# Kernel tuning notes

Hardware: AMD Instinct MI355X
Metric: run time of the kernel (lower is better)

## Reference

```python
import jax, jax.numpy as jnp
import numpy as np

B, N, D, H, L = 2, 2048, 512, 8, 2
HD = D // H


def setup_inputs() -> dict:
    key = jax.random.key(0)
    ks = jax.random.split(key, 8)
    s = 0.02
    return {
        "inputs_embeds": jax.random.normal(ks[0], (B, N, D), jnp.float32),
        "pos_emb": jax.random.normal(ks[1], (N, D), jnp.float32) * s,
        "c_attn_w": jax.random.normal(ks[2], (L, D, 3 * D), jnp.float32) * s,
        "c_attn_b": jnp.zeros((L, 3 * D), jnp.float32),
        "out_w": jax.random.normal(ks[3], (L, D, D), jnp.float32) * s,
        "out_b": jnp.zeros((L, D), jnp.float32),
        "ln1_g": jnp.ones((L, D), jnp.float32),
        "ln1_b": jnp.zeros((L, D), jnp.float32),
        "c_fc_w": jax.random.normal(ks[4], (L, D, 4 * D), jnp.float32) * s,
        "c_fc_b": jnp.zeros((L, 4 * D), jnp.float32),
        "c_proj_w": jax.random.normal(ks[5], (L, 4 * D, D), jnp.float32) * s,
        "c_proj_b": jnp.zeros((L, D), jnp.float32),
        "ln2_g": jnp.ones((L, D), jnp.float32),
        "ln2_b": jnp.zeros((L, D), jnp.float32),
    }


def _layernorm(x, g, b, eps=1e-5):
    mu = jnp.mean(x, axis=-1, keepdims=True)
    var = jnp.mean(jnp.square(x - mu), axis=-1, keepdims=True)
    return (x - mu) * jax.lax.rsqrt(var + eps) * g + b


def _gelu_new(x):
    # NewGELUActivation: tanh approximation
    return 0.5 * x * (1.0 + jnp.tanh(jnp.sqrt(2.0 / jnp.pi) * (x + 0.044715 * x ** 3)))


def _attention(x, w_qkv, b_qkv, w_out, b_out, self_mask):
    qkv = x @ w_qkv + b_qkv                      # [B,N,3D]
    q, k, v = jnp.split(qkv, 3, axis=-1)
    def heads(t):
        return t.reshape(B, N, H, HD).transpose(0, 2, 1, 3)  # [B,H,N,HD]
    q, k, v = heads(q), heads(k), heads(v)
    scores = jnp.einsum('bhqd,bhkd->bhqk', q, k) / jnp.sqrt(jnp.float32(HD))
    neg = jnp.finfo(scores.dtype).min
    scores = jnp.where(self_mask, scores, neg)   # exclude-self mask
    attn = jax.nn.softmax(scores, axis=-1)
    o = jnp.einsum('bhqk,bhkd->bhqd', attn, v)
    o = o.transpose(0, 2, 1, 3).reshape(B, N, D)
    return o @ w_out + b_out


def reference(inputs_embeds, pos_emb, c_attn_w, c_attn_b, out_w, out_b,
              ln1_g, ln1_b, c_fc_w, c_fc_b, c_proj_w, c_proj_b, ln2_g, ln2_b):
    self_mask = ~jnp.eye(N, dtype=bool)[None, None]  # [1,1,N,N]
    h = inputs_embeds + pos_emb[None]
    for l in range(L):
        res = h
        x = _layernorm(h, ln1_g[l], ln1_b[l])
        h = _attention(x, c_attn_w[l], c_attn_b[l], out_w[l], out_b[l], self_mask) + res
        res = h
        x = _layernorm(h, ln2_g[l], ln2_b[l])
        x = _gelu_new(x @ c_fc_w[l] + c_fc_b[l])
        h = (x @ c_proj_w[l] + c_proj_b[l]) + res
    return h
```

## Files before the change

kernel.cpp:

```cpp
#include <hip/hip_runtime.h>
#include <hip/hip_bf16.h>
#include <math.h>

#define BB 2
#define NN 2048
#define DD 512
#define HH 8
#define LL 2
#define TT (BB*NN)

typedef short short8 __attribute__((ext_vector_type(8)));
typedef float floatx4 __attribute__((ext_vector_type(4)));

__device__ __forceinline__ unsigned short f2b(float v) {
    union { float f; unsigned u; } x; x.f = v;
    unsigned r = x.u + 0x7fff + ((x.u >> 16) & 1);
    return (unsigned short)(r >> 16);
}

__global__ __launch_bounds__(256) void k_embed(const float* __restrict__ emb,
                                               const float* __restrict__ pos,
                                               float* __restrict__ h) {
    int i = blockIdx.x * 256 + threadIdx.x;
    h[i] = emb[i] + pos[i & (NN * DD - 1)];
}

__global__ __launch_bounds__(256) void k_ln(const float* __restrict__ hin,
                                            unsigned short* __restrict__ xout,
                                            const float* __restrict__ g,
                                            const float* __restrict__ b) {
    __shared__ float red[4];
    __shared__ float bc1, bc2;
    int t = blockIdx.x;
    int tid = threadIdx.x;
    int lane = tid & 63, wv = tid >> 6;
    const float* row = hin + (size_t)t * DD;
    float v0 = row[tid];
    float v1 = row[tid + 256];

    float s = v0 + v1;
#pragma unroll
    for (int o = 32; o; o >>= 1) s += __shfl_down(s, o, 64);
    if (lane == 0) red[wv] = s;
    __syncthreads();
    if (tid == 0) bc1 = (red[0] + red[1] + red[2] + red[3]) * (1.0f / DD);
    __syncthreads();
    float mu = bc1;
    float d0 = v0 - mu, d1 = v1 - mu;
    s = d0 * d0 + d1 * d1;
#pragma unroll
    for (int o = 32; o; o >>= 1) s += __shfl_down(s, o, 64);
    if (lane == 0) red[wv] = s;
    __syncthreads();
    if (tid == 0) bc2 = (red[0] + red[1] + red[2] + red[3]) * (1.0f / DD);
    __syncthreads();
    float rstd = rsqrtf(bc2 + 1e-5f);
    xout[(size_t)t * DD + tid]       = f2b(d0 * rstd * g[tid] + b[tid]);
    xout[(size_t)t * DD + tid + 256] = f2b(d1 * rstd * g[tid + 256] + b[tid + 256]);
}

__device__ __forceinline__ float gelu_new(float v) {
    const float c = 0.7978845608028654f;
    float u = c * (v + 0.044715f * v * v * v);
    return 0.5f * v * (1.0f + tanhf(u));
}

#define PL 3145728
__global__ __launch_bounds__(256) void k_wt_all(const float* __restrict__ c_attn_w,
                                                const float* __restrict__ out_w,
                                                const float* __restrict__ c_fc_w,
                                                const float* __restrict__ c_proj_w,
                                                unsigned short* __restrict__ wbuf) {
    __shared__ unsigned short t[64][72];
    int bx = blockIdx.x;
    int l = bx / 768;
    int r = bx - l * 768;
    const float* W; unsigned short* WT; int K, N;
    if (r < 192)      { W = c_attn_w + (size_t)l * 512 * 1536; WT = wbuf + (size_t)l * PL;           K = 512;  N = 1536; }
    else if (r < 256) { r -= 192; W = out_w  + (size_t)l * 512 * 512;  WT = wbuf + (size_t)l * PL + 786432;  K = 512;  N = 512; }
    else if (r < 512) { r -= 256; W = c_fc_w + (size_t)l * 512 * 2048; WT = wbuf + (size_t)l * PL + 1048576; K = 512;  N = 2048; }
    else              { r -= 512; W = c_proj_w + (size_t)l * 2048 * 512; WT = wbuf + (size_t)l * PL + 2097152; K = 2048; N = 512; }
    int tiles_n = N >> 6;
    int n0 = (r % tiles_n) * 64, k0 = (r / tiles_n) * 64;

    int tid = threadIdx.x;
    int rr = tid >> 2;
    int c0 = (tid & 3) * 16;
    const float* src = W + (size_t)(k0 + rr) * N + n0 + c0;
#pragma unroll
    for (int u = 0; u < 4; u++) {
        float4 v = *(const float4*)&src[u * 4];
        t[c0 + u * 4 + 0][rr] = f2b(v.x);
        t[c0 + u * 4 + 1][rr] = f2b(v.y);
        t[c0 + u * 4 + 2][rr] = f2b(v.z);
        t[c0 + u * 4 + 3][rr] = f2b(v.w);
    }
    __syncthreads();
    unsigned short* dst = WT + (size_t)(n0 + rr) * K + k0 + c0;
#pragma unroll
    for (int u = 0; u < 4; u++)
        *(uint2*)&dst[u * 4] = *(const uint2*)&t[rr][c0 + u * 4];
}

template <int ACT, int RES, int BF16OUT>
__global__ __launch_bounds__(256) void k_mgemm(const unsigned short* __restrict__ Ab,
                                               const unsigned short* __restrict__ Bt,
                                               const float* __restrict__ bias,
                                               const float* __restrict__ Rp,
                                               float* __restrict__ Cp,
                                               unsigned short* __restrict__ Cb,
                                               int K, int N) {
    __shared__ unsigned short Als[8 * 512];
    __shared__ unsigned short Bls[8 * 512];

    int tid = threadIdx.x;
    int l = tid & 63, w = tid >> 6;
    int wm = w >> 1, wn = w & 1;
    int m0 = blockIdx.y * 128, n0 = blockIdx.x * 128;
    int lr = l & 15;
    int lk = (l >> 4) * 8;

    const unsigned short* Ap0 = Ab + (size_t)(m0 + (w * 2 + 0) * 16 + lr) * K + lk;
    const unsigned short* Ap1 = Ab + (size_t)(m0 + (w * 2 + 1) * 16 + lr) * K + lk;
    const unsigned short* Bp0 = Bt + (size_t)(n0 + (w * 2 + 0) * 16 + lr) * K + lk;
    const unsigned short* Bp1 = Bt + (size_t)(n0 + (w * 2 + 1) * 16 + lr) * K + lk;

    floatx4 acc[4][4];
#pragma unroll
    for (int i = 0; i < 4; i++)
#pragma unroll
        for (int j = 0; j < 4; j++) acc[i][j] = (floatx4){0.f, 0.f, 0.f, 0.f};

    uint4 ra0 = *(const uint4*)Ap0;
    uint4 ra1 = *(const uint4*)Ap1;
    uint4 rb0 = *(const uint4*)Bp0;
    uint4 rb1 = *(const uint4*)Bp1;

    for (int k0 = 0; k0 < K; k0 += 32) {
        __syncthreads();
        *(uint4*)&Als[(w * 2 + 0) * 512 + l * 8] = ra0;
        *(uint4*)&Als[(w * 2 + 1) * 512 + l * 8] = ra1;
        *(uint4*)&Bls[(w * 2 + 0) * 512 + l * 8] = rb0;
        *(uint4*)&Bls[(w * 2 + 1) * 512 + l * 8] = rb1;
        __syncthreads();
        if (k0 + 32 < K) {
            ra0 = *(const uint4*)(Ap0 + k0 + 32);
            ra1 = *(const uint4*)(Ap1 + k0 + 32);
            rb0 = *(const uint4*)(Bp0 + k0 + 32);
            rb1 = *(const uint4*)(Bp1 + k0 + 32);
        }
        short8 a[4], b[4];
#pragma unroll
        for (int i = 0; i < 4; i++) {
            a[i] = *(const short8*)&Als[(wm * 4 + i) * 512 + l * 8];
            b[i] = *(const short8*)&Bls[(wn * 4 + i) * 512 + l * 8];
        }
#pragma unroll
        for (int i = 0; i < 4; i++)
#pragma unroll
            for (int j = 0; j < 4; j++)
                acc[i][j] = __builtin_amdgcn_mfma_f32_16x16x32_bf16(a[i], b[j], acc[i][j], 0, 0, 0);
    }

    int col_in = l & 15, rquad = (l >> 4) * 4;
#pragma unroll
    for (int i = 0; i < 4; i++) {
        int gm_base = m0 + wm * 64 + i * 16 + rquad;
#pragma unroll
        for (int j = 0; j < 4; j++) {
            int gn = n0 + wn * 64 + j * 16 + col_in;
            float bv = bias[gn];
#pragma unroll
            for (int r = 0; r < 4; r++) {
                size_t off = (size_t)(gm_base + r) * N + gn;
                float v = acc[i][j][r] + bv;
                if (ACT) v = gelu_new(v);
                if (RES) v += Rp[off];
                if (BF16OUT) Cb[off] = f2b(v);
                else Cp[off] = v;
            }
        }
    }
}

__global__ __launch_bounds__(256) void k_attn_mfma(const unsigned short* __restrict__ qkv,
                                                   unsigned short* __restrict__ xatt) {
    __shared__ unsigned short Ks[64 * 72];
    __shared__ unsigned short Vt[64 * 72];
    __shared__ unsigned short Pls[64 * 72];

    int qt = blockIdx.x, hd = blockIdx.y, b = blockIdx.z;
    int tid = threadIdx.x;
    int l = tid & 63, w = tid >> 6;
    int lr = l & 15, quad = l >> 4;

    const size_t base = (size_t)b * NN * 1536;

    short8 qf[2];
    {
        const unsigned short* qrow = qkv + base + (size_t)(qt * 64 + w * 16 + lr) * 1536 + hd * 64;
        qf[0] = *(const short8*)&qrow[quad * 8];
        qf[1] = *(const short8*)&qrow[quad * 8 + 32];
    }

    floatx4 O[4];
#pragma unroll
    for (int jd = 0; jd < 4; jd++) O[jd] = (floatx4){0.f, 0.f, 0.f, 0.f};
    float lsum[4] = {0.f, 0.f, 0.f, 0.f};

    int sr = tid >> 2, sc = (tid & 3) * 16;
    int vk = (tid & 15) * 4, vd = (tid >> 4) * 4;
    const unsigned short* Kbase = qkv + base + 512 + hd * 64;
    const unsigned short* Vbase = qkv + base + 1024 + hd * 64;

    uint4 rk0, rk1;
    union { uint2 u; unsigned short s[4]; } rv[4];
    rk0 = *(const uint4*)&Kbase[(size_t)sr * 1536 + sc];
    rk1 = *(const uint4*)&Kbase[(size_t)sr * 1536 + sc + 8];
#pragma unroll
    for (int i = 0; i < 4; i++)
        rv[i].u = *(const uint2*)&Vbase[(size_t)(vk + i) * 1536 + vd];

    for (int kt = 0; kt < 32; kt++) {
        __syncthreads();
        *(uint4*)&Ks[sr * 72 + sc]     = rk0;
        *(uint4*)&Ks[sr * 72 + sc + 8] = rk1;
#pragma unroll
        for (int j = 0; j < 4; j++) {
            union { uint2 u; unsigned short s[4]; } pk;
            pk.s[0] = rv[0].s[j]; pk.s[1] = rv[1].s[j];
            pk.s[2] = rv[2].s[j]; pk.s[3] = rv[3].s[j];
            *(uint2*)&Vt[(vd + j) * 72 + vk] = pk.u;
        }
        __syncthreads();
        if (kt < 31) {
            int kn = (kt + 1) * 64;
            rk0 = *(const uint4*)&Kbase[(size_t)(kn + sr) * 1536 + sc];
            rk1 = *(const uint4*)&Kbase[(size_t)(kn + sr) * 1536 + sc + 8];
#pragma unroll
            for (int i = 0; i < 4; i++)
                rv[i].u = *(const uint2*)&Vbase[(size_t)(kn + vk + i) * 1536 + vd];
        }

        floatx4 s[4];
#pragma unroll
        for (int jn = 0; jn < 4; jn++) s[jn] = (floatx4){0.f, 0.f, 0.f, 0.f};
#pragma unroll
        for (int ss = 0; ss < 2; ss++)
#pragma unroll
            for (int jn = 0; jn < 4; jn++) {
                short8 bk = *(const short8*)&Ks[(jn * 16 + lr) * 72 + ss * 32 + quad * 8];
                s[jn] = __builtin_amdgcn_mfma_f32_16x16x32_bf16(qf[ss], bk, s[jn], 0, 0, 0);
            }

        float p[4][4];
#pragma unroll
        for (int jn = 0; jn < 4; jn++)
#pragma unroll
            for (int r = 0; r < 4; r++)
                p[jn][r] = __expf(s[jn][r] * 0.125f - 8.0f);
        if (kt == qt) {
            int m_base = w * 16 + quad * 4;
#pragma unroll
            for (int jn = 0; jn < 4; jn++)
#pragma unroll
                for (int r = 0; r < 4; r++)
                    if (m_base + r == jn * 16 + lr) p[jn][r] = 0.0f;
        }
#pragma unroll
        for (int jn = 0; jn < 4; jn++)
#pragma unroll
            for (int r = 0; r < 4; r++) {
                lsum[r] += p[jn][r];
                Pls[(w * 16 + quad * 4 + r) * 72 + jn * 16 + lr] = f2b(p[jn][r]);
            }

#pragma unroll
        for (int ss = 0; ss < 2; ss++) {
            short8 ap = *(const short8*)&Pls[(w * 16 + lr) * 72 + ss * 32 + quad * 8];
#pragma unroll
            for (int jd = 0; jd < 4; jd++) {
                short8 bv = *(const short8*)&Vt[(jd * 16 + lr) * 72 + ss * 32 + quad * 8];
                O[jd] = __builtin_amdgcn_mfma_f32_16x16x32_bf16(ap, bv, O[jd], 0, 0, 0);
            }
        }
    }

#pragma unroll
    for (int r = 0; r < 4; r++) {
#pragma unroll
        for (int msk = 1; msk < 16; msk <<= 1) lsum[r] += __shfl_xor(lsum[r], msk);
    }
#pragma unroll
    for (int r = 0; r < 4; r++) {
        float inv = 1.0f / lsum[r];
        size_t tok = (size_t)b * NN + qt * 64 + w * 16 + quad * 4 + r;
#pragma unroll
        for (int jd = 0; jd < 4; jd++)
            xatt[tok * DD + hd * 64 + jd * 16 + lr] = f2b(O[jd][r] * inv);
    }
}

__global__ __launch_bounds__(256) void k_copy(const float* __restrict__ h,
                                              float* __restrict__ out) {
    int i = blockIdx.x * 256 + threadIdx.x;
    out[i] = h[i];
}

extern "C" void kernel_launch(void* const* d_in, const int* in_sizes, int n_in,
                              void* d_out, int out_size, void* d_ws, size_t ws_size,
                              hipStream_t stream) {
    const float* emb      = (const float*)d_in[0];
    const float* pos      = (const float*)d_in[1];
    const float* c_attn_w = (const float*)d_in[2];
    const float* c_attn_b = (const float*)d_in[3];
    const float* out_w    = (const float*)d_in[4];
    const float* out_b    = (const float*)d_in[5];
    const float* ln1_g    = (const float*)d_in[6];
    const float* ln1_b    = (const float*)d_in[7];
    const float* c_fc_w   = (const float*)d_in[8];
    const float* c_fc_b   = (const float*)d_in[9];
    const float* c_proj_w = (const float*)d_in[10];
    const float* c_proj_b = (const float*)d_in[11];
    const float* ln2_g    = (const float*)d_in[12];
    const float* ln2_b    = (const float*)d_in[13];

    char* p = (char*)d_ws;
    float* h = (float*)p;                       p += (size_t)TT * DD * 4;
    unsigned short* act = (unsigned short*)p;   p += (size_t)TT * 2048 * 2;
    unsigned short* x = (unsigned short*)p;     p += (size_t)TT * DD * 2;
    unsigned short* xatt = (unsigned short*)p;  p += (size_t)TT * DD * 2;
    unsigned short* wbuf = (unsigned short*)p;

    unsigned short* qkvb = act;
    unsigned short* ffa  = act;
    float* out = (float*)d_out;

    k_embed<<<TT * DD / 256, 256, 0, stream>>>(emb, pos, h);
    k_wt_all<<<1536, 256, 0, stream>>>(c_attn_w, out_w, c_fc_w, c_proj_w, wbuf);

    for (int l = 0; l < LL; l++) {
        unsigned short* wqkv_t  = wbuf + (size_t)l * PL;
        unsigned short* wout_t  = wqkv_t + 786432;
        unsigned short* wfc_t   = wqkv_t + 1048576;
        unsigned short* wproj_t = wqkv_t + 2097152;

        k_ln<<<TT, 256, 0, stream>>>(h, x, ln1_g + l * DD, ln1_b + l * DD);
        k_mgemm<0, 0, 1><<<dim3(1536 / 128, TT / 128), 256, 0, stream>>>(
            x, wqkv_t, c_attn_b + l * 1536, nullptr, nullptr, qkvb, 512, 1536);
        k_attn_mfma<<<dim3(NN / 64, HH, BB), 256, 0, stream>>>(qkvb, xatt);
        k_mgemm<0, 1, 0><<<dim3(512 / 128, TT / 128), 256, 0, stream>>>(
            xatt, wout_t, out_b + l * 512, h, h, nullptr, 512, 512);
        k_ln<<<TT, 256, 0, stream>>>(h, x, ln2_g + l * DD, ln2_b + l * DD);
        k_mgemm<1, 0, 1><<<dim3(2048 / 128, TT / 128), 256, 0, stream>>>(
            x, wfc_t, c_fc_b + l * 2048, nullptr, nullptr, ffa, 512, 2048);
        k_mgemm<0, 1, 0><<<dim3(512 / 128, TT / 128), 256, 0, stream>>>(
            ffa, wproj_t, c_proj_b + l * 512, h, h, nullptr, 2048, 512);
    }

    k_copy<<<TT * DD / 256, 256, 0, stream>>>(h, out);
}
```

Before: 442.8 us.

## Double-buffer GEMM LDS with async loads, transpose attention scores, drop final copy

The GEMM mainloop now uses two LDS buffers. It prefetches the next K-slice straight into LDS with global_load_lds when that builtin exists, so each iteration needs one barrier instead of two and skips the register staging. The attention kernel computes the scores as K·Qᵀ, so each lane holds one query row. That lets P be written to LDS with vectorized stores and cuts the row-sum reduction to two shuffles. The last layer's projection GEMM writes directly to the output buffer, which removes the separate copy kernel. The main risk is whether the async LDS loads are correctly waited on before the barrier.

Result: slower. 462.2 us (+4.4%).

```diff
diff --git a/kernel.cpp b/kernel.cpp
--- a/kernel.cpp
+++ b/kernel.cpp
@@ -17,6 +17,17 @@
     unsigned r = x.u + 0x7fff + ((x.u >> 16) & 1);
     return (unsigned short)(r >> 16);
 }
+
+#if __has_builtin(__builtin_amdgcn_global_load_lds)
+#define HAVE_ASYNC 1
+__device__ __forceinline__ void g2l16(const void* g, void* l) {
+    __builtin_amdgcn_global_load_lds(
+        (const __attribute__((address_space(1))) unsigned int*)g,
+        (__attribute__((address_space(3))) unsigned int*)l, 16, 0, 0);
+}
+#else
+#define HAVE_ASYNC 0
+#endif
 
 __global__ __launch_bounds__(256) void k_embed(const float* __restrict__ emb,
                                                const float* __restrict__ pos,
@@ -110,8 +121,8 @@
                                                float* __restrict__ Cp,
                                                unsigned short* __restrict__ Cb,
                                                int K, int N) {
-    __shared__ unsigned short Als[8 * 512];
-    __shared__ unsigned short Bls[8 * 512];
+    __shared__ unsigned short Als[2][8 * 512];
+    __shared__ unsigned short Bls[2][8 * 512];
 
     int tid = threadIdx.x;
     int l = tid & 63, w = tid >> 6;
@@ -124,6 +135,8 @@
     const unsigned short* Ap1 = Ab + (size_t)(m0 + (w * 2 + 1) * 16 + lr) * K + lk;
     const unsigned short* Bp0 = Bt + (size_t)(n0 + (w * 2 + 0) * 16 + lr) * K + lk;
     const unsigned short* Bp1 = Bt + (size_t)(n0 + (w * 2 + 1) * 16 + lr) * K + lk;
+    int la0 = (w * 2 + 0) * 512 + l * 8;
+    int la1 = (w * 2 + 1) * 512 + l * 8;
 
     floatx4 acc[4][4];
 #pragma unroll
@@ -131,29 +144,41 @@
 #pragma unroll
         for (int j = 0; j < 4; j++) acc[i][j] = (floatx4){0.f, 0.f, 0.f, 0.f};
 
-    uint4 ra0 = *(const uint4*)Ap0;
-    uint4 ra1 = *(const uint4*)Ap1;
-    uint4 rb0 = *(const uint4*)Bp0;
-    uint4 rb1 = *(const uint4*)Bp1;
-
-    for (int k0 = 0; k0 < K; k0 += 32) {
+#if HAVE_ASYNC
+    g2l16(Ap0, &Als[0][la0]);
+    g2l16(Ap1, &Als[0][la1]);
+    g2l16(Bp0, &Bls[0][la0]);
+    g2l16(Bp1, &Bls[0][la1]);
+#else
+    *(uint4*)&Als[0][la0] = *(const uint4*)Ap0;
+    *(uint4*)&Als[0][la1] = *(const uint4*)Ap1;
+    *(uint4*)&Bls[0][la0] = *(const uint4*)Bp0;
+    *(uint4*)&Bls[0][la1] = *(const uint4*)Bp1;
+#endif
+
+    int nit = K >> 5;
+    for (int it = 0; it < nit; it++) {
+        int cur = it & 1;
         __syncthreads();
-        *(uint4*)&Als[(w * 2 + 0) * 512 + l * 8] = ra0;
-        *(uint4*)&Als[(w * 2 + 1) * 512 + l * 8] = ra1;
-        *(uint4*)&Bls[(w * 2 + 0) * 512 + l * 8] = rb0;
-        *(uint4*)&Bls[(w * 2 + 1) * 512 + l * 8] = rb1;
-        __syncthreads();
-        if (k0 + 32 < K) {
-            ra0 = *(const uint4*)(Ap0 + k0 + 32);
-            ra1 = *(const uint4*)(Ap1 + k0 + 32);
-            rb0 = *(const uint4*)(Bp0 + k0 + 32);
-            rb1 = *(const uint4*)(Bp1 + k0 + 32);
+        if (it + 1 < nit) {
+            int ko = (it + 1) << 5;
+#if HAVE_ASYNC
+            g2l16(Ap0 + ko, &Als[cur ^ 1][la0]);
+            g2l16(Ap1 + ko, &Als[cur ^ 1][la1]);
+            g2l16(Bp0 + ko, &Bls[cur ^ 1][la0]);
+            g2l16(Bp1 + ko, &Bls[cur ^ 1][la1]);
+#else
+            *(uint4*)&Als[cur ^ 1][la0] = *(const uint4*)(Ap0 + ko);
+            *(uint4*)&Als[cur ^ 1][la1] = *(const uint4*)(Ap1 + ko);
+            *(uint4*)&Bls[cur ^ 1][la0] = *(const uint4*)(Bp0 + ko);
+            *(uint4*)&Bls[cur ^ 1][la1] = *(const uint4*)(Bp1 + ko);
+#endif
         }
         short8 a[4], b[4];
 #pragma unroll
         for (int i = 0; i < 4; i++) {
-            a[i] = *(const short8*)&Als[(wm * 4 + i) * 512 + l * 8];
-            b[i] = *(const short8*)&Bls[(wn * 4 + i) * 512 + l * 8];
+            a[i] = *(const short8*)&Als[cur][(wm * 4 + i) * 512 + l * 8];
+            b[i] = *(const short8*)&Bls[cur][(wn * 4 + i) * 512 + l * 8];
         }
 #pragma unroll
         for (int i = 0; i < 4; i++)
@@ -206,7 +231,7 @@
     floatx4 O[4];
 #pragma unroll
     for (int jd = 0; jd < 4; jd++) O[jd] = (floatx4){0.f, 0.f, 0.f, 0.f};
-    float lsum[4] = {0.f, 0.f, 0.f, 0.f};
+    float lsum = 0.0f;
 
     int sr = tid >> 2, sc = (tid & 3) * 16;
     int vk = (tid & 15) * 4, vd = (tid >> 4) * 4;
@@ -249,31 +274,23 @@
         for (int ss = 0; ss < 2; ss++)
 #pragma unroll
             for (int jn = 0; jn < 4; jn++) {
-                short8 bk = *(const short8*)&Ks[(jn * 16 + lr) * 72 + ss * 32 + quad * 8];
-                s[jn] = __builtin_amdgcn_mfma_f32_16x16x32_bf16(qf[ss], bk, s[jn], 0, 0, 0);
+                short8 ak = *(const short8*)&Ks[(jn * 16 + lr) * 72 + ss * 32 + quad * 8];
+                s[jn] = __builtin_amdgcn_mfma_f32_16x16x32_bf16(ak, qf[ss], s[jn], 0, 0, 0);
             }
 
-        float p[4][4];
-#pragma unroll
-        for (int jn = 0; jn < 4; jn++)
-#pragma unroll
-            for (int r = 0; r < 4; r++)
-                p[jn][r] = __expf(s[jn][r] * 0.125f - 8.0f);
-        if (kt == qt) {
-            int m_base = w * 16 + quad * 4;
-#pragma unroll
-            for (int jn = 0; jn < 4; jn++)
-#pragma unroll
-                for (int r = 0; r < 4; r++)
-                    if (m_base + r == jn * 16 + lr) p[jn][r] = 0.0f;
-        }
-#pragma unroll
-        for (int jn = 0; jn < 4; jn++)
+        int mq = w * 16 + lr;
+#pragma unroll
+        for (int jn = 0; jn < 4; jn++) {
+            union { uint2 u; unsigned short h[4]; } pk;
 #pragma unroll
             for (int r = 0; r < 4; r++) {
-                lsum[r] += p[jn][r];
-                Pls[(w * 16 + quad * 4 + r) * 72 + jn * 16 + lr] = f2b(p[jn][r]);
+                float p = __expf(s[jn][r] * 0.125f - 8.0f);
+                if (kt == qt && mq == jn * 16 + quad * 4 + r) p = 0.0f;
+                lsum += p;
+                pk.h[r] = f2b(p);
             }
+            *(uint2*)&Pls[mq * 72 + jn * 16 + quad * 4] = pk.u;
+        }
 
 #pragma unroll
         for (int ss = 0; ss < 2; ss++) {
@@ -286,25 +303,16 @@
         }
     }
 
+    lsum += __shfl_xor(lsum, 16);
+    lsum += __shfl_xor(lsum, 32);
 #pragma unroll
     for (int r = 0; r < 4; r++) {
-#pragma unroll
-        for (int msk = 1; msk < 16; msk <<= 1) lsum[r] += __shfl_xor(lsum[r], msk);
-    }
-#pragma unroll
-    for (int r = 0; r < 4; r++) {
-        float inv = 1.0f / lsum[r];
+        float inv = 1.0f / __shfl(lsum, quad * 4 + r, 16);
         size_t tok = (size_t)b * NN + qt * 64 + w * 16 + quad * 4 + r;
 #pragma unroll
         for (int jd = 0; jd < 4; jd++)
             xatt[tok * DD + hd * 64 + jd * 16 + lr] = f2b(O[jd][r] * inv);
     }
-}
-
-__global__ __launch_bounds__(256) void k_copy(const float* __restrict__ h,
-                                              float* __restrict__ out) {
-    int i = blockIdx.x * 256 + threadIdx.x;
-    out[i] = h[i];
 }
 
 extern "C" void kernel_launch(void* const* d_in, const int* in_sizes, int n_in,
@@ -344,6 +352,7 @@
         unsigned short* wout_t  = wqkv_t + 786432;
         unsigned short* wfc_t   = wqkv_t + 1048576;
         unsigned short* wproj_t = wqkv_t + 2097152;
+        float* proj_dst = (l == LL - 1) ? out : h;
 
         k_ln<<<TT, 256, 0, stream>>>(h, x, ln1_g + l * DD, ln1_b + l * DD);
         k_mgemm<0, 0, 1><<<dim3(1536 / 128, TT / 128), 256, 0, stream>>>(
@@ -355,8 +364,6 @@
         k_mgemm<1, 0, 1><<<dim3(2048 / 128, TT / 128), 256, 0, stream>>>(
             x, wfc_t, c_fc_b + l * 2048, nullptr, nullptr, ffa, 512, 2048);
         k_mgemm<0, 1, 0><<<dim3(512 / 128, TT / 128), 256, 0, stream>>>(
-            ffa, wproj_t, c_proj_b + l * 512, h, h, nullptr, 2048, 512);
-    }
-
-    k_copy<<<TT * DD / 256, 256, 0, stream>>>(h, out);
-}
+            ffa, wproj_t, c_proj_b + l * 512, h, proj_dst, nullptr, 2048, 512);
+    }
+}
```

## Split-K the narrow GEMMs with atomic accumulation and vectorize attention P stores

Applied to the files above, without the earlier changes.

The out-projection and FFN down-projection GEMMs (N=512, only 128 blocks) now split K across grid z (2 and 4 chunks) and atomically add partial sums into the residual buffer. A separate bias-add kernel pre-seeds the destination with residual plus bias. The last layer writes straight to the output, which removes the final copy kernel. The attention QK MFMA operands are swapped so each lane holds four consecutive keys, which allows packed 64-bit P stores and a cheaper row-sum reduction. This adds float atomics, an extra elementwise pass per GEMM, and non-deterministic summation order.

After: 450.3 us. About the same (+1.7%).

```diff
diff --git a/kernel.cpp b/kernel.cpp
--- a/kernel.cpp
+++ b/kernel.cpp
@@ -23,6 +23,13 @@
                                                float* __restrict__ h) {
     int i = blockIdx.x * 256 + threadIdx.x;
     h[i] = emb[i] + pos[i & (NN * DD - 1)];
+}
+
+__global__ __launch_bounds__(256) void k_bias_add(const float* __restrict__ src,
+                                                  const float* __restrict__ bias,
+                                                  float* __restrict__ dst) {
+    int i = blockIdx.x * 256 + threadIdx.x;
+    dst[i] = src[i] + bias[i & (DD - 1)];
 }
 
 __global__ __launch_bounds__(256) void k_ln(const float* __restrict__ hin,
@@ -102,14 +109,14 @@
         *(uint2*)&dst[u * 4] = *(const uint2*)&t[rr][c0 + u * 4];
 }
 
-template <int ACT, int RES, int BF16OUT>
+template <int ACT, int RES, int BF16OUT, int ATOMIC>
 __global__ __launch_bounds__(256) void k_mgemm(const unsigned short* __restrict__ Ab,
                                                const unsigned short* __restrict__ Bt,
                                                const float* __restrict__ bias,
                                                const float* __restrict__ Rp,
                                                float* __restrict__ Cp,
                                                unsigned short* __restrict__ Cb,
-                                               int K, int N) {
+                                               int Kfull, int Kchunk, int N) {
     __shared__ unsigned short Als[8 * 512];
     __shared__ unsigned short Bls[8 * 512];
 
@@ -117,13 +124,14 @@
     int l = tid & 63, w = tid >> 6;
     int wm = w >> 1, wn = w & 1;
     int m0 = blockIdx.y * 128, n0 = blockIdx.x * 128;
+    int kb = blockIdx.z * Kchunk;
     int lr = l & 15;
     int lk = (l >> 4) * 8;
 
-    const unsigned short* Ap0 = Ab + (size_t)(m0 + (w * 2 + 0) * 16 + lr) * K + lk;
-    const unsigned short* Ap1 = Ab + (size_t)(m0 + (w * 2 + 1) * 16 + lr) * K + lk;
-    const unsigned short* Bp0 = Bt + (size_t)(n0 + (w * 2 + 0) * 16 + lr) * K + lk;
-    const unsigned short* Bp1 = Bt + (size_t)(n0 + (w * 2 + 1) * 16 + lr) * K + lk;
+    const unsigned short* Ap0 = Ab + (size_t)(m0 + (w * 2 + 0) * 16 + lr) * Kfull + kb + lk;
+    const unsigned short* Ap1 = Ab + (size_t)(m0 + (w * 2 + 1) * 16 + lr) * Kfull + kb + lk;
+    const unsigned short* Bp0 = Bt + (size_t)(n0 + (w * 2 + 0) * 16 + lr) * Kfull + kb + lk;
+    const unsigned short* Bp1 = Bt + (size_t)(n0 + (w * 2 + 1) * 16 + lr) * Kfull + kb + lk;
 
     floatx4 acc[4][4];
 #pragma unroll
@@ -136,14 +144,14 @@
     uint4 rb0 = *(const uint4*)Bp0;
     uint4 rb1 = *(const uint4*)Bp1;
 
-    for (int k0 = 0; k0 < K; k0 += 32) {
+    for (int k0 = 0; k0 < Kchunk; k0 += 32) {
         __syncthreads();
         *(uint4*)&Als[(w * 2 + 0) * 512 + l * 8] = ra0;
         *(uint4*)&Als[(w * 2 + 1) * 512 + l * 8] = ra1;
         *(uint4*)&Bls[(w * 2 + 0) * 512 + l * 8] = rb0;
         *(uint4*)&Bls[(w * 2 + 1) * 512 + l * 8] = rb1;
         __syncthreads();
-        if (k0 + 32 < K) {
+        if (k0 + 32 < Kchunk) {
             ra0 = *(const uint4*)(Ap0 + k0 + 32);
             ra1 = *(const uint4*)(Ap1 + k0 + 32);
             rb0 = *(const uint4*)(Bp0 + k0 + 32);
@@ -169,15 +177,19 @@
 #pragma unroll
         for (int j = 0; j < 4; j++) {
             int gn = n0 + wn * 64 + j * 16 + col_in;
-            float bv = bias[gn];
+            float bv = ATOMIC ? 0.0f : bias[gn];
 #pragma unroll
             for (int r = 0; r < 4; r++) {
                 size_t off = (size_t)(gm_base + r) * N + gn;
-                float v = acc[i][j][r] + bv;
-                if (ACT) v = gelu_new(v);
-                if (RES) v += Rp[off];
-                if (BF16OUT) Cb[off] = f2b(v);
-                else Cp[off] = v;
+                if (ATOMIC) {
+                    atomicAdd(&Cp[off], acc[i][j][r]);
+                } else {
+                    float v = acc[i][j][r] + bv;
+                    if (ACT) v = gelu_new(v);
+                    if (RES) v += Rp[off];
+                    if (BF16OUT) Cb[off] = f2b(v);
+                    else Cp[off] = v;
+                }
             }
         }
     }
@@ -206,7 +218,7 @@
     floatx4 O[4];
 #pragma unroll
     for (int jd = 0; jd < 4; jd++) O[jd] = (floatx4){0.f, 0.f, 0.f, 0.f};
-    float lsum[4] = {0.f, 0.f, 0.f, 0.f};
+    float lsum = 0.0f;
 
     int sr = tid >> 2, sc = (tid & 3) * 16;
     int vk = (tid & 15) * 4, vd = (tid >> 4) * 4;
@@ -249,31 +261,23 @@
         for (int ss = 0; ss < 2; ss++)
 #pragma unroll
             for (int jn = 0; jn < 4; jn++) {
-                short8 bk = *(const short8*)&Ks[(jn * 16 + lr) * 72 + ss * 32 + quad * 8];
-                s[jn] = __builtin_amdgcn_mfma_f32_16x16x32_bf16(qf[ss], bk, s[jn], 0, 0, 0);
+                short8 ak = *(const short8*)&Ks[(jn * 16 + lr) * 72 + ss * 32 + quad * 8];
+                s[jn] = __builtin_amdgcn_mfma_f32_16x16x32_bf16(ak, qf[ss], s[jn], 0, 0, 0);
             }
 
-        float p[4][4];
-#pragma unroll
-        for (int jn = 0; jn < 4; jn++)
-#pragma unroll
-            for (int r = 0; r < 4; r++)
-                p[jn][r] = __expf(s[jn][r] * 0.125f - 8.0f);
-        if (kt == qt) {
-            int m_base = w * 16 + quad * 4;
-#pragma unroll
-            for (int jn = 0; jn < 4; jn++)
-#pragma unroll
-                for (int r = 0; r < 4; r++)
-                    if (m_base + r == jn * 16 + lr) p[jn][r] = 0.0f;
-        }
-#pragma unroll
-        for (int jn = 0; jn < 4; jn++)
+        int mq = w * 16 + lr;
+#pragma unroll
+        for (int jn = 0; jn < 4; jn++) {
+            union { uint2 u; unsigned short h[4]; } pk;
 #pragma unroll
             for (int r = 0; r < 4; r++) {
-                lsum[r] += p[jn][r];
-                Pls[(w * 16 + quad * 4 + r) * 72 + jn * 16 + lr] = f2b(p[jn][r]);
+                float p = __expf(s[jn][r] * 0.125f - 8.0f);
+                if (kt == qt && mq == jn * 16 + quad * 4 + r) p = 0.0f;
+                lsum += p;
+                pk.h[r] = f2b(p);
             }
+            *(uint2*)&Pls[mq * 72 + jn * 16 + quad * 4] = pk.u;
+        }
 
 #pragma unroll
         for (int ss = 0; ss < 2; ss++) {
@@ -286,25 +290,16 @@
         }
     }
 
+    lsum += __shfl_xor(lsum, 16);
+    lsum += __shfl_xor(lsum, 32);
 #pragma unroll
     for (int r = 0; r < 4; r++) {
-#pragma unroll
-        for (int msk = 1; msk < 16; msk <<= 1) lsum[r] += __shfl_xor(lsum[r], msk);
-    }
-#pragma unroll
-    for (int r = 0; r < 4; r++) {
-        float inv = 1.0f / lsum[r];
+        float inv = 1.0f / __shfl(lsum, quad * 4 + r, 16);
         size_t tok = (size_t)b * NN + qt * 64 + w * 16 + quad * 4 + r;
 #pragma unroll
         for (int jd = 0; jd < 4; jd++)
             xatt[tok * DD + hd * 64 + jd * 16 + lr] = f2b(O[jd][r] * inv);
     }
-}
-
-__global__ __launch_bounds__(256) void k_copy(const float* __restrict__ h,
-                                              float* __restrict__ out) {
-    int i = blockIdx.x * 256 + threadIdx.x;
-    out[i] = h[i];
 }
 
 extern "C" void kernel_launch(void* const* d_in, const int* in_sizes, int n_in,
@@ -344,19 +339,20 @@
         unsigned short* wout_t  = wqkv_t + 786432;
         unsigned short* wfc_t   = wqkv_t + 1048576;
         unsigned short* wproj_t = wqkv_t + 2097152;
+        float* proj_dst = (l == LL - 1) ? out : h;
 
         k_ln<<<TT, 256, 0, stream>>>(h, x, ln1_g + l * DD, ln1_b + l * DD);
-        k_mgemm<0, 0, 1><<<dim3(1536 / 128, TT / 128), 256, 0, stream>>>(
-            x, wqkv_t, c_attn_b + l * 1536, nullptr, nullptr, qkvb, 512, 1536);
+        k_mgemm<0, 0, 1, 0><<<dim3(1536 / 128, TT / 128), 256, 0, stream>>>(
+            x, wqkv_t, c_attn_b + l * 1536, nullptr, nullptr, qkvb, 512, 512, 1536);
         k_attn_mfma<<<dim3(NN / 64, HH, BB), 256, 0, stream>>>(qkvb, xatt);
-        k_mgemm<0, 1, 0><<<dim3(512 / 128, TT / 128), 256, 0, stream>>>(
-            xatt, wout_t, out_b + l * 512, h, h, nullptr, 512, 512);
+        k_bias_add<<<TT * DD / 256, 256, 0, stream>>>(h, out_b + l * DD, h);
+        k_mgemm<0, 0, 0, 1><<<dim3(512 / 128, TT / 128, 2), 256, 0, stream>>>(
+            xatt, wout_t, nullptr, nullptr, h, nullptr, 512, 256, 512);
         k_ln<<<TT, 256, 0, stream>>>(h, x, ln2_g + l * DD, ln2_b + l * DD);
-        k_mgemm<1, 0, 1><<<dim3(2048 / 128, TT / 128), 256, 0, stream>>>(
-            x, wfc_t, c_fc_b + l * 2048, nullptr, nullptr, ffa, 512, 2048);
-        k_mgemm<0, 1, 0><<<dim3(512 / 128, TT / 128), 256, 0, stream>>>(
-            ffa, wproj_t, c_proj_b + l * 512, h, h, nullptr, 2048, 512);
-    }
-
-    k_copy<<<TT * DD / 256, 256, 0, stream>>>(h, out);
-}
+        k_mgemm<1, 0, 1, 0><<<dim3(2048 / 128, TT / 128), 256, 0, stream>>>(
+            x, wfc_t, c_fc_b + l * 2048, nullptr, nullptr, ffa, 512, 512, 2048);
+        k_bias_add<<<TT * DD / 256, 256, 0, stream>>>(h, c_proj_b + l * DD, proj_dst);
+        k_mgemm<0, 0, 0, 1><<<dim3(512 / 128, TT / 128, 4), 256, 0, stream>>>(
+            ffa, wproj_t, nullptr, nullptr, proj_dst, nullptr, 2048, 512, 512);
+    }
+}
```
